# Kernel optimization log

Hardware: AMD Instinct MI355X
Metric: run time of the kernel (lower is better)

The kernel has to match this reference:

```python
import jax, jax.numpy as jnp
import numpy as np

N = 131072      # total nodes per branch
G = 4096        # graphs in batch
NPG = 32        # nodes per graph
E = 1048576     # edges per branch (avg degree 8)
S = 64          # state_size
H = 128         # hidden_size
OUT = 1         # out_size
NEG_SLOPE = 0.2


def _make_edges(key):
    k1, k2, k3 = jax.random.split(key, 3)
    base = jax.random.randint(k1, (E,), 0, G) * NPG
    src = base + jax.random.randint(k2, (E,), 0, NPG)
    dst = base + jax.random.randint(k3, (E,), 0, NPG)
    return jnp.stack([src, dst]).astype(jnp.int64)


def setup_inputs() -> dict:
    key = jax.random.key(0)
    ks = jax.random.split(key, 12)
    batch = (jnp.arange(N) // NPG).astype(jnp.int64)
    return {
        "up_x": jax.random.normal(ks[0], (N, S), jnp.float32),
        "up_edge_index": _make_edges(ks[1]),
        "up_batch": batch,
        "down_x": jax.random.normal(ks[2], (N, S), jnp.float32),
        "down_edge_index": _make_edges(ks[3]),
        "down_batch": batch,
        "up_W": jax.random.normal(ks[4], (S, H), jnp.float32) / np.sqrt(S),
        "up_att_src": jax.random.normal(ks[5], (H,), jnp.float32) / np.sqrt(H),
        "up_att_dst": jax.random.normal(ks[6], (H,), jnp.float32) / np.sqrt(H),
        "up_bias": jnp.zeros((H,), jnp.float32),
        "down_W": jax.random.normal(ks[7], (S, H), jnp.float32) / np.sqrt(S),
        "down_att_src": jax.random.normal(ks[8], (H,), jnp.float32) / np.sqrt(H),
        "down_att_dst": jax.random.normal(ks[9], (H,), jnp.float32) / np.sqrt(H),
        "down_bias": jnp.zeros((H,), jnp.float32),
        "mlp_W": jax.random.normal(ks[10], (H, OUT), jnp.float32) / np.sqrt(H),
        "mlp_b": jnp.zeros((OUT,), jnp.float32),
    }


def _gat_conv(x, edge_index, W, att_src, att_dst, bias):
    # PyG GATConv, heads=1, add_self_loops=False
    h = x @ W                                  # [N, H]
    src, dst = edge_index[0], edge_index[1]
    a_src = h @ att_src                        # [N]
    a_dst = h @ att_dst                        # [N]
    e = jax.nn.leaky_relu(a_src[src] + a_dst[dst], NEG_SLOPE)  # [E]
    # segment softmax over incoming edges of each dst node
    m = jax.ops.segment_max(e, dst, num_segments=N)
    p = jnp.exp(e - m[dst])
    denom = jax.ops.segment_sum(p, dst, num_segments=N)
    alpha = p / (denom[dst] + 1e-16)
    out = jax.ops.segment_sum(alpha[:, None] * h[src], dst, num_segments=N)
    return out + bias


def _branch(x, edge_index, batch, W, att_src, att_dst, bias):
    h = _gat_conv(x, edge_index, W, att_src, att_dst, bias)
    num_nodes = jax.ops.segment_sum(jnp.ones_like(batch), batch, num_segments=G)
    self_idx = jnp.cumsum(num_nodes) - 1       # last node of each graph
    return jax.nn.sigmoid(h[self_idx])         # [G, H]


def reference(up_x, up_edge_index, up_batch, down_x, down_edge_index, down_batch,
              up_W, up_att_src, up_att_dst, up_bias,
              down_W, down_att_src, down_att_dst, down_bias,
              mlp_W, mlp_b):
    up = _branch(up_x, up_edge_index, up_batch, up_W, up_att_src, up_att_dst, up_bias)
    down = _branch(down_x, down_edge_index, down_batch, down_W, down_att_src, down_att_dst, down_bias)
    x = up * down
    return x @ mlp_W + mlp_b                   # [G, OUT]
```

## Files before the change

kernel.cpp:

```cpp
#include <hip/hip_runtime.h>
#include <math.h>

#define G_GRAPHS 4096
#define NPG 32
#define E_EDGES 1048576
#define S_DIM 64
#define H_DIM 128
#define CAP 128
#define MAXIT 8
#define NEG_SLOPE 0.2f


__global__ __launch_bounds__(256) void init_kernel(
        int* __restrict__ cnt, float* __restrict__ wvec,
        const float* __restrict__ upW, const float* __restrict__ upAs,
        const float* __restrict__ upAd,
        const float* __restrict__ dnW, const float* __restrict__ dnAs,
        const float* __restrict__ dnAd) {
    int t = threadIdx.x;
    for (int i = t; i < 2 * G_GRAPHS; i += 256) cnt[i] = 0;
    int vec = t >> 6;
    int s   = t & 63;
    const float* W   = (vec < 2) ? upW : dnW;
    const float* att = (vec == 0) ? upAs : (vec == 1) ? upAd : (vec == 2) ? dnAs : dnAd;
    const float4* Wr = (const float4*)(W + s * H_DIM);
    const float4* A4 = (const float4*)att;
    float a0 = 0.f, a1 = 0.f, a2 = 0.f, a3 = 0.f;
    #pragma unroll
    for (int h = 0; h < H_DIM / 4; ++h) {
        float4 w = Wr[h], a = A4[h];
        a0 += w.x * a.x; a1 += w.y * a.y; a2 += w.z * a.z; a3 += w.w * a.w;
    }
    wvec[vec * 64 + s] = (a0 + a1) + (a2 + a3);
}

__global__ __launch_bounds__(256) void scan_kernel(
        const int* __restrict__ up_ei, const int* __restrict__ dn_ei,
        int* __restrict__ cnt, int* __restrict__ buckets) {
    int branch = blockIdx.y;
    const int* ei = branch ? dn_ei : up_ei;
    unsigned e4 = blockIdx.x * 256u + threadIdx.x;
    int4 d4 = ((const int4*)(ei + E_EDGES))[e4];
    int* bcnt  = cnt + branch * G_GRAPHS;
    int* bbase = buckets + branch * G_GRAPHS * CAP;
    unsigned e0 = e4 * 4u;
    int ds[4] = {d4.x, d4.y, d4.z, d4.w};
    #pragma unroll
    for (int j = 0; j < 4; ++j) {
        int dst = ds[j];
        if ((dst & (NPG - 1)) == NPG - 1) {
            int g = dst >> 5;
            int pos = atomicAdd(bcnt + g, 1);
            if (pos < CAP) bbase[g * CAP + pos] = ei[e0 + j];
        }
    }
}

__global__ __launch_bounds__(128) void gat_kernel(
        const float* __restrict__ up_x, const float* __restrict__ dn_x,
        const float* __restrict__ upW, const float* __restrict__ dnW,
        const float* __restrict__ up_bias, const float* __restrict__ dn_bias,
        const float* __restrict__ mlp_W, const float* __restrict__ mlp_b,
        const int* __restrict__ cnt, const int* __restrict__ buckets,
        const float* __restrict__ wvec, float* __restrict__ out) {
    int g    = blockIdx.x;
    int wave = threadIdx.x >> 6;
    int lane = threadIdx.x & 63;
    int q    = lane >> 4;
    int t    = lane & 15;

    __shared__ float evals[2][CAP];
    __shared__ float xsum_s[2][S_DIM];
    __shared__ float bout[2][H_DIM];

    const float*  x    = wave ? dn_x : up_x;
    const float4* x4   = (const float4*)x;
    const float*  W    = wave ? dnW : upW;
    const float*  bias = wave ? dn_bias : up_bias;
    const float*  wsrc = wvec + wave * 128;
    const float4  ws4  = ((const float4*)wsrc)[t];
    const float4  wd4  = ((const float4*)(wsrc + 64))[t];

    int d = g * NPG + (NPG - 1);

    float4 xd = x4[d * 16 + t];
    float ad = xd.x * wd4.x + xd.y * wd4.y + xd.z * wd4.z + xd.w * wd4.w;
    #pragma unroll
    for (int m = 1; m < 16; m <<= 1) ad += __shfl_xor(ad, m, 64);

    int k = cnt[wave * G_GRAPHS + g];
    if (k > CAP) k = CAP;
    const int* bk = buckets + (wave * G_GRAPHS + g) * CAP;
    int kk = (k + 3) >> 2;

    float4 rows[MAXIT];
    #pragma unroll
    for (int it = 0; it < MAXIT; ++it) {
        if (it >= kk) break;
        int i = it * 4 + q;
        bool valid = (i < k);
        int src = bk[valid ? i : 0];
        float4 xr = x4[src * 16 + t];
        rows[it] = xr;
        float e = xr.x * ws4.x + xr.y * ws4.y + xr.z * ws4.z + xr.w * ws4.w;
        #pragma unroll
        for (int m = 1; m < 16; m <<= 1) e += __shfl_xor(e, m, 64);
        e += ad;
        e = (e > 0.f) ? e : NEG_SLOPE * e;
        if (valid && t == 0) evals[wave][i] = e;
    }
    for (int it = MAXIT; it < kk; ++it) {
        int i = it * 4 + q;
        bool valid = (i < k);
        int src = bk[valid ? i : 0];
        float4 xr = x4[src * 16 + t];
        float e = xr.x * ws4.x + xr.y * ws4.y + xr.z * ws4.z + xr.w * ws4.w;
        #pragma unroll
        for (int m = 1; m < 16; m <<= 1) e += __shfl_xor(e, m, 64);
        e += ad;
        e = (e > 0.f) ? e : NEG_SLOPE * e;
        if (valid && t == 0) evals[wave][i] = e;
    }

    float mmax = -INFINITY;
    for (int i = lane; i < k; i += 64) mmax = fmaxf(mmax, evals[wave][i]);
    #pragma unroll
    for (int m = 32; m; m >>= 1) mmax = fmaxf(mmax, __shfl_xor(mmax, m, 64));
    float denom = 0.f;
    for (int i = lane; i < k; i += 64) {
        float p = __expf(evals[wave][i] - mmax);
        evals[wave][i] = p;
        denom += p;
    }
    #pragma unroll
    for (int m = 32; m; m >>= 1) denom += __shfl_xor(denom, m, 64);
    float inv = 1.f / (denom + 1e-16f);

    float4 acc = {0.f, 0.f, 0.f, 0.f};
    #pragma unroll
    for (int it = 0; it < MAXIT; ++it) {
        if (it >= kk) break;
        int i = it * 4 + q;
        float p = (i < k) ? evals[wave][i] : 0.f;
        float4 xr = rows[it];
        acc.x += p * xr.x; acc.y += p * xr.y; acc.z += p * xr.z; acc.w += p * xr.w;
    }
    for (int it = MAXIT; it < kk; ++it) {
        int i = it * 4 + q;
        bool valid = (i < k);
        float p = valid ? evals[wave][i] : 0.f;
        int src = bk[valid ? i : 0];
        float4 xr = x4[src * 16 + t];
        acc.x += p * xr.x; acc.y += p * xr.y; acc.z += p * xr.z; acc.w += p * xr.w;
    }
    #pragma unroll
    for (int m = 16; m < 64; m <<= 1) {
        acc.x += __shfl_xor(acc.x, m, 64);
        acc.y += __shfl_xor(acc.y, m, 64);
        acc.z += __shfl_xor(acc.z, m, 64);
        acc.w += __shfl_xor(acc.w, m, 64);
    }
    if (lane < 16) {
        float4 xs = {acc.x * inv, acc.y * inv, acc.z * inv, acc.w * inv};
        ((float4*)xsum_s[wave])[lane] = xs;
    }

    const float2* W2 = (const float2*)W;
    float2 bb = ((const float2*)bias)[lane];
    float o0 = bb.x, o1 = bb.y;
    #pragma unroll 8
    for (int s = 0; s < S_DIM; ++s) {
        float xv = xsum_s[wave][s];
        float2 w = W2[s * 64 + lane];
        o0 += xv * w.x;
        o1 += xv * w.y;
    }
    o0 = 1.f / (1.f + __expf(-o0));
    o1 = 1.f / (1.f + __expf(-o1));
    bout[wave][2 * lane]     = o0;
    bout[wave][2 * lane + 1] = o1;
    __syncthreads();

    if (wave == 0) {
        float2 u  = ((const float2*)bout[0])[lane];
        float2 dn = ((const float2*)bout[1])[lane];
        float2 mw = ((const float2*)mlp_W)[lane];
        float part = u.x * dn.x * mw.x + u.y * dn.y * mw.y;
        #pragma unroll
        for (int m = 32; m; m >>= 1) part += __shfl_xor(part, m, 64);
        if (lane == 0) out[g] = part + mlp_b[0];
    }
}

extern "C" void kernel_launch(void* const* d_in, const int* in_sizes, int n_in,
                              void* d_out, int out_size, void* d_ws, size_t ws_size,
                              hipStream_t stream) {
    const float* up_x  = (const float*)d_in[0];
    const int*   up_ei = (const int*)d_in[1];
    const float* dn_x  = (const float*)d_in[3];
    const int*   dn_ei = (const int*)d_in[4];
    const float* upW   = (const float*)d_in[6];
    const float* upAs  = (const float*)d_in[7];
    const float* upAd  = (const float*)d_in[8];
    const float* upB   = (const float*)d_in[9];
    const float* dnW   = (const float*)d_in[10];
    const float* dnAs  = (const float*)d_in[11];
    const float* dnAd  = (const float*)d_in[12];
    const float* dnB   = (const float*)d_in[13];
    const float* mlpW  = (const float*)d_in[14];
    const float* mlpB  = (const float*)d_in[15];
    float* out = (float*)d_out;

    int*   cnt     = (int*)d_ws;
    int*   buckets = cnt + 2 * G_GRAPHS;
    float* wvec    = (float*)(buckets + 2 * G_GRAPHS * CAP);

    init_kernel<<<1, 256, 0, stream>>>(cnt, wvec, upW, upAs, upAd, dnW, dnAs, dnAd);
    scan_kernel<<<dim3(E_EDGES / 4 / 256, 2), 256, 0, stream>>>(up_ei, dn_ei, cnt, buckets);
    gat_kernel<<<G_GRAPHS, 128, 0, stream>>>(up_x, dn_x, upW, dnW, upB, dnB,
                                             mlpW, mlpB, cnt, buckets, wvec, out);
}
```

Before: 155.4 us.

## Split per-graph GAT into gather kernel and batched register-tiled head GEMM kernel

The fused per-graph kernel is split in two. The gather kernel now writes the attention-weighted feature sums to a global workspace. A new head kernel then processes 64 graphs per block, staging their sums in padded shared memory and running a register-tiled 64x128 projection, followed by the sigmoid, the product of the two branches and the MLP. This lets each block reuse the W loads across many graphs instead of re-reading W once per graph, at the cost of an extra launch and a global round trip for the intermediate sums. The counter zeroing in the init kernel is also vectorized.

```diff
diff --git a/kernel.cpp b/kernel.cpp
--- a/kernel.cpp
+++ b/kernel.cpp
@@ -9,6 +9,8 @@
 #define CAP 128
 #define MAXIT 8
 #define NEG_SLOPE 0.2f
+#define GPB 64
+#define LDP 68
 
 
 __global__ __launch_bounds__(256) void init_kernel(
@@ -18,7 +20,9 @@
         const float* __restrict__ dnW, const float* __restrict__ dnAs,
         const float* __restrict__ dnAd) {
     int t = threadIdx.x;
-    for (int i = t; i < 2 * G_GRAPHS; i += 256) cnt[i] = 0;
+    int4 z = {0, 0, 0, 0};
+    #pragma unroll
+    for (int i = 0; i < 8; ++i) ((int4*)cnt)[t + 256 * i] = z;
     int vec = t >> 6;
     int s   = t & 63;
     const float* W   = (vec < 2) ? upW : dnW;
@@ -56,13 +60,10 @@
     }
 }
 
-__global__ __launch_bounds__(128) void gat_kernel(
+__global__ __launch_bounds__(128) void gather_kernel(
         const float* __restrict__ up_x, const float* __restrict__ dn_x,
-        const float* __restrict__ upW, const float* __restrict__ dnW,
-        const float* __restrict__ up_bias, const float* __restrict__ dn_bias,
-        const float* __restrict__ mlp_W, const float* __restrict__ mlp_b,
         const int* __restrict__ cnt, const int* __restrict__ buckets,
-        const float* __restrict__ wvec, float* __restrict__ out) {
+        const float* __restrict__ wvec, float* __restrict__ xsum) {
     int g    = blockIdx.x;
     int wave = threadIdx.x >> 6;
     int lane = threadIdx.x & 63;
@@ -70,13 +71,8 @@
     int t    = lane & 15;
 
     __shared__ float evals[2][CAP];
-    __shared__ float xsum_s[2][S_DIM];
-    __shared__ float bout[2][H_DIM];
-
-    const float*  x    = wave ? dn_x : up_x;
-    const float4* x4   = (const float4*)x;
-    const float*  W    = wave ? dnW : upW;
-    const float*  bias = wave ? dn_bias : up_bias;
+
+    const float4* x4   = (const float4*)(wave ? dn_x : up_x);
     const float*  wsrc = wvec + wave * 128;
     const float4  ws4  = ((const float4*)wsrc)[t];
     const float4  wd4  = ((const float4*)(wsrc + 64))[t];
@@ -162,33 +158,99 @@
     }
     if (lane < 16) {
         float4 xs = {acc.x * inv, acc.y * inv, acc.z * inv, acc.w * inv};
-        ((float4*)xsum_s[wave])[lane] = xs;
-    }
-
-    const float2* W2 = (const float2*)W;
-    float2 bb = ((const float2*)bias)[lane];
-    float o0 = bb.x, o1 = bb.y;
-    #pragma unroll 8
-    for (int s = 0; s < S_DIM; ++s) {
-        float xv = xsum_s[wave][s];
-        float2 w = W2[s * 64 + lane];
-        o0 += xv * w.x;
-        o1 += xv * w.y;
-    }
-    o0 = 1.f / (1.f + __expf(-o0));
-    o1 = 1.f / (1.f + __expf(-o1));
-    bout[wave][2 * lane]     = o0;
-    bout[wave][2 * lane + 1] = o1;
+        ((float4*)(xsum + (size_t)(wave * G_GRAPHS + g) * S_DIM))[lane] = xs;
+    }
+}
+
+__global__ __launch_bounds__(256) void head_kernel(
+        const float* __restrict__ upW, const float* __restrict__ dnW,
+        const float* __restrict__ up_bias, const float* __restrict__ dn_bias,
+        const float* __restrict__ mlp_W, const float* __restrict__ mlp_b,
+        const float* __restrict__ xsum, float* __restrict__ out) {
+    int g0  = blockIdx.x * GPB;
+    int tid = threadIdx.x;
+    int hp  = tid & 15;
+    int gg  = tid >> 4;
+
+    __shared__ float xsu[GPB * LDP];
+    __shared__ float xsd[GPB * LDP];
+    const float4* xu4 = (const float4*)(xsum + (size_t)g0 * S_DIM);
+    const float4* xd4 = (const float4*)(xsum + (size_t)(G_GRAPHS + g0) * S_DIM);
+    #pragma unroll
+    for (int i = 0; i < 4; ++i) {
+        int idx = tid + 256 * i;
+        int row = idx >> 4, c4 = idx & 15;
+        ((float4*)(xsu + row * LDP))[c4] = xu4[idx];
+        ((float4*)(xsd + row * LDP))[c4] = xd4[idx];
+    }
     __syncthreads();
 
-    if (wave == 0) {
-        float2 u  = ((const float2*)bout[0])[lane];
-        float2 dn = ((const float2*)bout[1])[lane];
-        float2 mw = ((const float2*)mlp_W)[lane];
-        float part = u.x * dn.x * mw.x + u.y * dn.y * mw.y;
-        #pragma unroll
-        for (int m = 32; m; m >>= 1) part += __shfl_xor(part, m, 64);
-        if (lane == 0) out[g] = part + mlp_b[0];
+    float4 au[4][2] = {};
+    float4 av[4][2] = {};
+    const float4* Wu4 = (const float4*)upW;
+    const float4* Wd4 = (const float4*)dnW;
+
+    for (int s4 = 0; s4 < S_DIM / 4; ++s4) {
+        float4 xu[4], xv[4];
+        #pragma unroll
+        for (int j = 0; j < 4; ++j) {
+            int g = gg * 4 + j;
+            xu[j] = ((const float4*)(xsu + g * LDP))[s4];
+            xv[j] = ((const float4*)(xsd + g * LDP))[s4];
+        }
+        #pragma unroll
+        for (int c = 0; c < 4; ++c) {
+            int s = s4 * 4 + c;
+            #pragma unroll
+            for (int p = 0; p < 2; ++p) {
+                float4 wu = Wu4[s * 32 + hp + 16 * p];
+                float4 wd = Wd4[s * 32 + hp + 16 * p];
+                #pragma unroll
+                for (int j = 0; j < 4; ++j) {
+                    float a = (c == 0) ? xu[j].x : (c == 1) ? xu[j].y
+                            : (c == 2) ? xu[j].z : xu[j].w;
+                    float b = (c == 0) ? xv[j].x : (c == 1) ? xv[j].y
+                            : (c == 2) ? xv[j].z : xv[j].w;
+                    au[j][p].x += a * wu.x; au[j][p].y += a * wu.y;
+                    au[j][p].z += a * wu.z; au[j][p].w += a * wu.w;
+                    av[j][p].x += b * wd.x; av[j][p].y += b * wd.y;
+                    av[j][p].z += b * wd.z; av[j][p].w += b * wd.w;
+                }
+            }
+        }
+    }
+
+    float4 bu[2], bd[2], mw[2];
+    #pragma unroll
+    for (int p = 0; p < 2; ++p) {
+        bu[p] = ((const float4*)up_bias)[hp + 16 * p];
+        bd[p] = ((const float4*)dn_bias)[hp + 16 * p];
+        mw[p] = ((const float4*)mlp_W)[hp + 16 * p];
+    }
+    float mb = mlp_b[0];
+
+    #pragma unroll
+    for (int j = 0; j < 4; ++j) {
+        float hsum = 0.f;
+        #pragma unroll
+        for (int p = 0; p < 2; ++p) {
+            float uo, dv;
+            uo = 1.f / (1.f + __expf(-(au[j][p].x + bu[p].x)));
+            dv = 1.f / (1.f + __expf(-(av[j][p].x + bd[p].x)));
+            hsum += uo * dv * mw[p].x;
+            uo = 1.f / (1.f + __expf(-(au[j][p].y + bu[p].y)));
+            dv = 1.f / (1.f + __expf(-(av[j][p].y + bd[p].y)));
+            hsum += uo * dv * mw[p].y;
+            uo = 1.f / (1.f + __expf(-(au[j][p].z + bu[p].z)));
+            dv = 1.f / (1.f + __expf(-(av[j][p].z + bd[p].z)));
+            hsum += uo * dv * mw[p].z;
+            uo = 1.f / (1.f + __expf(-(au[j][p].w + bu[p].w)));
+            dv = 1.f / (1.f + __expf(-(av[j][p].w + bd[p].w)));
+            hsum += uo * dv * mw[p].w;
+        }
+        #pragma unroll
+        for (int m = 1; m < 16; m <<= 1) hsum += __shfl_xor(hsum, m, 64);
+        if (hp == 0) out[g0 + gg * 4 + j] = hsum + mb;
     }
 }
 
@@ -214,9 +276,11 @@
     int*   cnt     = (int*)d_ws;
     int*   buckets = cnt + 2 * G_GRAPHS;
     float* wvec    = (float*)(buckets + 2 * G_GRAPHS * CAP);
+    float* xsum    = wvec + 4 * 64;
 
     init_kernel<<<1, 256, 0, stream>>>(cnt, wvec, upW, upAs, upAd, dnW, dnAs, dnAd);
     scan_kernel<<<dim3(E_EDGES / 4 / 256, 2), 256, 0, stream>>>(up_ei, dn_ei, cnt, buckets);
-    gat_kernel<<<G_GRAPHS, 128, 0, stream>>>(up_x, dn_x, upW, dnW, upB, dnB,
-                                             mlpW, mlpB, cnt, buckets, wvec, out);
-}
+    gather_kernel<<<G_GRAPHS, 128, 0, stream>>>(up_x, dn_x, cnt, buckets, wvec, xsum);
+    head_kernel<<<G_GRAPHS / GPB, 256, 0, stream>>>(upW, dnW, upB, dnB, mlpW, mlpB,
+                                                    xsum, out);
+}
```

Result: slower. 167.2 us (+7.6%).
